# Kernel optimization log

Hardware: AMD Instinct MI355X
Metric: run time of the kernel (lower is better)

## Reference

```python
import jax, jax.numpy as jnp
import numpy as np

D_MODEL = 256
SEQ_L = 4096
BATCH = 8
H = 3 * D_MODEL   # inner width after 3-branch concat
N_STATE = 32      # complex conjugate pairs -> d_state=64 real
KSIZES = (3, 7, 15)
DILATIONS = (1, 2, 4)


def setup_inputs() -> dict:
    k = jax.random.split(jax.random.key(0), 16)
    d = D_MODEL
    def w(ki, shape, scale):
        return jax.random.normal(ki, shape, jnp.float32) * scale
    inp = {"x": jax.random.normal(k[0], (BATCH, SEQ_L, d), jnp.float32)}
    for i, ksz in enumerate(KSIZES):
        inp[f"conv_w{i}"] = w(k[1 + i], (d, d, ksz), (d * ksz) ** -0.5)
        inp[f"conv_b{i}"] = jnp.zeros((d,), jnp.float32)
    inp["gate_w"] = w(k[4], (H, d), d ** -0.5)
    inp["gate_b"] = jnp.zeros((H,), jnp.float32)
    inp["res_w"] = w(k[5], (H, d), d ** -0.5)
    inp["res_b"] = jnp.zeros((H,), jnp.float32)
    # S4D (diagonal SSM) parameters, d_state=64 -> 32 complex pairs
    inp["log_dt"] = jax.random.uniform(k[6], (H,), jnp.float32, np.log(0.001), np.log(0.1))
    inp["A_re"] = -0.5 * jnp.ones((H, N_STATE), jnp.float32)
    inp["A_im"] = jnp.broadcast_to(np.pi * jnp.arange(N_STATE, dtype=jnp.float32), (H, N_STATE)).copy()
    inp["C_re"] = w(k[7], (H, N_STATE), 0.2)
    inp["C_im"] = w(k[8], (H, N_STATE), 0.2)
    inp["Dskip"] = jax.random.normal(k[9], (H,), jnp.float32)
    inp["ln_gamma"] = jnp.ones((H,), jnp.float32)
    inp["ln_beta"] = jnp.zeros((H,), jnp.float32)
    return inp


def _dil_conv(u, w, b, dil):
    # u: [B, C, L], w: [O, I, K], torch 'same' padding (odd kernels)
    y = jax.lax.conv_general_dilated(
        u, w, window_strides=(1,), padding="SAME", rhs_dilation=(dil,),
        dimension_numbers=("NCH", "OIH", "NCH"))
    return y + b[None, :, None]


def _s4d_apply(u, log_dt, A_re, A_im, C_re, C_im, Dskip):
    # u: [B, H, L]; diagonal SSM long convolution via FFT (ZOH discretization)
    L = u.shape[-1]
    dt = jnp.exp(log_dt)                          # [H]
    A = A_re + 1j * A_im                          # [H, N]
    C = C_re + 1j * C_im                          # [H, N]
    dtA = dt[:, None] * A                         # [H, N]
    C_disc = C * (jnp.exp(dtA) - 1.0) / A         # ZOH input matrix folded into C
    t = jnp.arange(L, dtype=jnp.float32)
    vand = jnp.exp(dtA[:, :, None] * t)           # [H, N, L] Vandermonde
    kern = 2.0 * jnp.real(jnp.einsum("hn,hnl->hl", C_disc, vand))  # [H, L]
    n_fft = 2 * L
    kf = jnp.fft.rfft(kern, n_fft)                # [H, n_fft/2+1]
    uf = jnp.fft.rfft(u, n_fft)                   # [B, H, n_fft/2+1]
    y = jnp.fft.irfft(uf * kf[None], n_fft)[..., :L]
    return y + Dskip[None, :, None] * u


def reference(x, conv_w0, conv_b0, conv_w1, conv_b1, conv_w2, conv_b2,
              gate_w, gate_b, res_w, res_b,
              log_dt, A_re, A_im, C_re, C_im, Dskip, ln_gamma, ln_beta):
    u = jnp.transpose(x, (0, 2, 1))               # [B, d, L]
    convs = [
        _dil_conv(u, conv_w0, conv_b0, DILATIONS[0]),
        _dil_conv(u, conv_w1, conv_b1, DILATIONS[1]),
        _dil_conv(u, conv_w2, conv_b2, DILATIONS[2]),
    ]
    combined = jnp.concatenate(convs, axis=1)     # [B, 3d, L]
    gate = jax.nn.sigmoid(jnp.einsum("bdl,od->bol", u, gate_w) + gate_b[None, :, None])
    gated = combined * gate
    s4_out = _s4d_apply(gated, log_dt, A_re, A_im, C_re, C_im, Dskip)
    resid = jnp.einsum("bdl,od->bol", u, res_w) + res_b[None, :, None]
    out = jnp.transpose(s4_out + resid, (0, 2, 1))  # [B, L, 3d]
    mu = jnp.mean(out, axis=-1, keepdims=True)
    var = jnp.mean((out - mu) ** 2, axis=-1, keepdims=True)
    return (out - mu) * jax.lax.rsqrt(var + 1e-5) * ln_gamma + ln_beta
```

## Files before the change

### kernel.cpp

```cpp
#include <hip/hip_runtime.h>
#include <cstdint>
#include <cstddef>


#define B_ 8
#define L_ 4096
#define D_ 256
#define H_ 768
#define NST 32
#define LC 128
#define NC 32

typedef _Float16 f16;
typedef _Float16 f16x8 __attribute__((ext_vector_type(8)));
typedef _Float16 f16x4 __attribute__((ext_vector_type(4)));
typedef _Float16 f16x2 __attribute__((ext_vector_type(2)));
typedef float f32x4 __attribute__((ext_vector_type(4)));

__device__ __forceinline__ f32x4 mfma16(f16x8 a, f16x8 b, f32x4 c) {
  return __builtin_amdgcn_mfma_f32_16x16x32_f16(a, b, c, 0, 0, 0);
}

#define GLDS16(g, l)                                                              \
  __builtin_amdgcn_global_load_lds((const __attribute__((address_space(1))) void*)(g), \
                                   (__attribute__((address_space(3))) void*)(l), 16, 0, 0)

__global__ __launch_bounds__(256) void prep_all(
    const float* __restrict__ x, const float* __restrict__ gate_w,
    const float* __restrict__ res_w,
    const float* __restrict__ w0, const float* __restrict__ w1, const float* __restrict__ w2,
    f16* __restrict__ xh, f16* __restrict__ Ag, float* __restrict__ zbuf,
    f16* __restrict__ A) {
  int bid = blockIdx.x, tid = threadIdx.x;
  if (bid < 8192) {
    int i = (bid * 256 + tid) * 4;
    float4 v = *(const float4*)(x + i);
    xh[i+0]=(f16)v.x; xh[i+1]=(f16)v.y; xh[i+2]=(f16)v.z; xh[i+3]=(f16)v.w;
  } else if (bid < 8384) {
    int i = ((bid - 8192) * 256 + tid) * 4;
    float4 v = *(const float4*)(gate_w + i);
    Ag[i+0]=(f16)v.x; Ag[i+1]=(f16)v.y; Ag[i+2]=(f16)v.z; Ag[i+3]=(f16)v.w;
  } else if (bid < 8576) {
    int i = ((bid - 8384) * 256 + tid) * 4;
    float4 v = *(const float4*)(res_w + i);
    f16* d = Ag + 768 * 256;
    d[i+0]=(f16)v.x; d[i+1]=(f16)v.y; d[i+2]=(f16)v.z; d[i+3]=(f16)v.w;
  } else if (bid == 8576) {
    zbuf[tid] = 0.f;
  } else {
    int idx = (bid - 8577) * 256 + tid;
    const int n0 = 256 * 256 * 3, n1 = 256 * 256 * 7;
    const float* w; int K, base;
    if (idx < n0) { w = w0; K = 3; base = 0; }
    else if (idx < n0 + n1) { idx -= n0; w = w1; K = 7; base = 256 * 768; }
    else { idx -= n0 + n1; w = w2; K = 15; base = 256 * 768 + 256 * 1792; }
    int o = idx / (256 * K); int r = idx - o * (256 * K); int j = r / K; int t = r - j * K;
    A[base + o * (256 * K) + t * 256 + j] = (f16)w[idx];
  }
}

__global__ __launch_bounds__(256) void s4_all(const float* __restrict__ log_dt,
                                              const float* __restrict__ A_re,
                                              const float* __restrict__ A_im,
                                              const float* __restrict__ C_re,
                                              const float* __restrict__ C_im,
                                              f16* __restrict__ A1, f16* __restrict__ A2,
                                              float* __restrict__ WLc,
                                              float* __restrict__ kT) {
  int bid = blockIdx.x, tid = threadIdx.x;
  if (bid < 96) {
    int idx = bid * 256 + tid;
    int h = idx >> 5, n = idx & 31;
    float dt = expf(log_dt[h]);
    float Ar = A_re[idx], Ai = A_im[idx];
    float ar = dt * Ar, ai = dt * Ai;
    float e = expf(ar), sn, cs; sincosf(ai, &sn, &cs);
    float wr = e * cs, wi = e * sn;
    float den = Ar * Ar + Ai * Ai;
    float Er = wr - 1.f, Ei = wi;
    float Cr = C_re[idx], Ci = C_im[idx];
    float nr = Cr * Er - Ci * Ei, ni = Cr * Ei + Ci * Er;
    float Cdr = (nr * Ar + ni * Ai) / den;
    float Cdi = (ni * Ar - nr * Ai) / den;
    f16* A1r = A1 + ((size_t)h * 64 + 2 * n) * LC;
    f16* A1i = A1 + ((size_t)h * 64 + 2 * n + 1) * LC;
    float pr = 1.f, pi = 0.f;
    for (int j = 0; j < LC; ++j) {
      A1r[LC - 1 - j] = (f16)pr; A1i[LC - 1 - j] = (f16)pi;
      float t0 = pr * wr - pi * wi; pi = pr * wi + pi * wr; pr = t0;
    }
    WLc[idx * 2] = pr; WLc[idx * 2 + 1] = pi;
    float qr = wr, qi = wi;
    for (int t = 0; t < LC; ++t) {
      A2[((size_t)h * LC + t) * 64 + 2 * n]     = (f16)(2.f * (Cdr * qr - Cdi * qi));
      A2[((size_t)h * LC + t) * 64 + 2 * n + 1] = (f16)(-2.f * (Cdr * qi + Cdi * qr));
      float t0 = qr * wr - qi * wi; qi = qr * wi + qi * wr; qr = t0;
    }
  } else {
    int idx = (bid - 96) * 256 + tid;
    int h = idx >> 7, j = idx & 127;
    float dt = expf(log_dt[h]);
    float acc = 0.f;
    for (int n = 0; n < NST; ++n) {
      float Ar = A_re[h * 32 + n], Ai = A_im[h * 32 + n];
      float ar = dt * Ar, ai = dt * Ai;
      float e1 = expf(ar), s1, c1; sincosf(ai, &s1, &c1);
      float wr = e1 * c1, wi = e1 * s1;
      float den = Ar * Ar + Ai * Ai;
      float Er = wr - 1.f, Ei = wi;
      float Cr = C_re[h * 32 + n], Ci = C_im[h * 32 + n];
      float nr = Cr * Er - Ci * Ei, ni = Cr * Ei + Ci * Er;
      float Cdr = (nr * Ar + ni * Ai) / den, Cdi = (ni * Ar - nr * Ai) / den;
      float ej = expf(ar * (float)j), sj, cj; sincosf(ai * (float)j, &sj, &cj);
      acc += 2.f * (Cdr * (ej * cj) - Cdi * (ej * sj));
    }
    kT[idx] = acc;
  }
}

__global__ __launch_bounds__(256) void gemm_gr(
    const f16* __restrict__ xh, const f16* __restrict__ Agr,
    const float* __restrict__ gate_b, const float* __restrict__ res_b,
    f16* __restrict__ gts, f16* __restrict__ res) {
  __shared__ f16 As[128 * 64];
  __shared__ f16 Bs[128 * 64];
  const int mt = blockIdx.y, nt = blockIdx.x;
  const int b = nt >> 5, l0 = (nt & 31) * 128;
  const bool isg = mt < 6;
  const int hbase = (isg ? mt : mt - 6) * 128;
  const f16* Abase = Agr + (size_t)((isg ? 0 : 768) + hbase) * 256;
  const int tid = threadIdx.x;
  const int wid = tid >> 6, lane = tid & 63, l15 = lane & 15, quad = lane >> 4;
  const int wm = (wid & 1) * 64, wn = (wid >> 1) * 64;
  const int srow = (wid << 5) + (lane >> 3);
  const int sperm = ((lane & 7) ^ (lane >> 3)) << 3;
  char* AsL = (char*)As + (wid << 12);
  char* BsL = (char*)Bs + (wid << 12);
  const f16* xrow = xh + (((size_t)b * L_) << 8);

  f32x4 acc[4][4];
#pragma unroll
  for (int i = 0; i < 4; ++i)
#pragma unroll
    for (int j = 0; j < 4; ++j) acc[i][j] = (f32x4){0.f, 0.f, 0.f, 0.f};

  for (int kc = 0; kc < 4; ++kc) {
#pragma unroll
    for (int j = 0; j < 4; ++j) {
      int row = srow + j * 8;
      GLDS16(Abase + (size_t)row * 256 + kc * 64 + sperm, AsL + (j << 10));
      GLDS16(xrow + ((size_t)(l0 + row) << 8) + kc * 64 + sperm, BsL + (j << 10));
    }
    __syncthreads();
#pragma unroll
    for (int k2 = 0; k2 < 2; ++k2) {
      f16x8 af[4], bf[4];
#pragma unroll
      for (int mi = 0; mi < 4; ++mi) {
        int r = wm + mi * 16 + l15;
        af[mi] = *(const f16x8*)(&As[r * 64 + (((k2 * 4 + quad) ^ (r & 7)) << 3)]);
      }
#pragma unroll
      for (int ni = 0; ni < 4; ++ni) {
        int r = wn + ni * 16 + l15;
        bf[ni] = *(const f16x8*)(&Bs[r * 64 + (((k2 * 4 + quad) ^ (r & 7)) << 3)]);
      }
#pragma unroll
      for (int mi = 0; mi < 4; ++mi)
#pragma unroll
        for (int ni = 0; ni < 4; ++ni) acc[mi][ni] = mfma16(af[mi], bf[ni], acc[mi][ni]);
    }
    __syncthreads();
  }

  if (isg) {
#pragma unroll
    for (int mi = 0; mi < 4; ++mi)
#pragma unroll
      for (int ni = 0; ni < 4; ++ni) {
        int hg = hbase + wm + mi * 16 + quad * 4;
        int lg = l0 + wn + ni * 16 + l15;
#pragma unroll
        for (int r = 0; r < 4; ++r) {
          float val = acc[mi][ni][r] + gate_b[hg + r];
          gts[((size_t)(b * H_ + hg + r)) * L_ + lg] = (f16)(1.f / (1.f + expf(-val)));
        }
      }
  } else {
#pragma unroll
    for (int mi = 0; mi < 4; ++mi)
#pragma unroll
      for (int ni = 0; ni < 4; ++ni) {
        int hg = hbase + wm + mi * 16 + quad * 4;
        int lg = l0 + wn + ni * 16 + l15;
#pragma unroll
        for (int r = 0; r < 4; ++r)
          res[((size_t)(b * H_ + hg + r)) * L_ + lg] = (f16)(acc[mi][ni][r] + res_b[hg + r]);
      }
  }
}

__global__ __launch_bounds__(512, 2) void gemm_conv8(
    const f16* __restrict__ xh, const f16* __restrict__ Aconv,
    const float* __restrict__ cb0, const float* __restrict__ cb1, const float* __restrict__ cb2,
    const f16* __restrict__ gts, const f16* __restrict__ zbuf,
    f16* __restrict__ v) {
  __shared__ f16 lds[65536];
  f16* A0 = lds;
  f16* B0 = lds + 16384;
  f16* A1 = lds + 32768;
  f16* B1 = lds + 49152;

  const int nt = blockIdx.x;
  const int b = nt >> 4, l0 = (nt & 15) * 256;
  const int ci = 2 - blockIdx.y;
  const int tid = threadIdx.x;
  const int wid = tid >> 6, lane = tid & 63, l15 = lane & 15, quad = lane >> 4;
  const int wr = wid >> 2, wc = wid & 3;
  const int r0 = tid >> 3;
  const int cswz = ((tid & 7) ^ ((tid >> 3) & 7)) << 3;
  const int rsw = lane & 7;
  const f16* xrow = xh + (((size_t)b * L_) << 8);

  const f16* Acb; int Krow, taps, dil;
  if (ci == 0)      { Acb = Aconv;                          Krow = 768;  taps = 3;  dil = 1; }
  else if (ci == 1) { Acb = Aconv + 256 * 768;              Krow = 1792; taps = 7;  dil = 2; }
  else              { Acb = Aconv + 256 * 768 + 256 * 1792; Krow = 3840; taps = 15; dil = 4; }
  const int KS = taps * 4;

  f32x4 acc[8][4];
#pragma unroll
  for (int i = 0; i < 8; ++i)
#pragma unroll
    for (int j = 0; j < 4; ++j) acc[i][j] = (f32x4){0.f, 0.f, 0.f, 0.f};
  f16x8 af[4][2], blo[2][2], bhi[2][2];

  auto stageA = [&](int kst, int h, f16* Ad) {
    int t = kst >> 2, jb = (kst & 3) << 6;
    const f16* s0 = Acb + (size_t)(h * 128 + r0) * Krow + t * 256 + jb + cswz;
    GLDS16(s0, Ad + h * 8192 + wid * 512);
    GLDS16(s0 + (size_t)64 * Krow, Ad + h * 8192 + 4096 + wid * 512);
  };
  auto stageB = [&](int kst, int h, f16* Bd) {
    int t = kst >> 2, jb = (kst & 3) << 6;
    int boff = (t - (taps - 1) / 2) * dil;
    int gl0 = l0 + h * 128 + r0 + boff;
    const f16* s0 = (gl0 < 0 || gl0 >= L_) ? (zbuf + cswz)
                    : xrow + ((size_t)gl0 << 8) + jb + cswz;
    GLDS16(s0, Bd + h * 8192 + wid * 512);
    int gl1 = gl0 + 64;
    const f16* s1 = (gl1 < 0 || gl1 >= L_) ? (zbuf + cswz)
                    : xrow + ((size_t)gl1 << 8) + jb + cswz;
    GLDS16(s1, Bd + h * 8192 + 4096 + wid * 512);
  };
  auto loadA = [&](const f16* Ab, int MH) {
#pragma unroll
    for (int mi = 0; mi < 4; ++mi) {
      int r = MH * 128 + wr * 64 + mi * 16 + l15;
#pragma unroll
      for (int k2 = 0; k2 < 2; ++k2)
        af[mi][k2] = *(const f16x8*)(Ab + r * 64 + (((k2 * 4 + quad) ^ rsw) << 3));
    }
  };
  auto loadB = [&](const f16* Bb, int NH, f16x8 (&bf)[2][2]) {
#pragma unroll
    for (int ni = 0; ni < 2; ++ni) {
      int r = NH * 128 + wc * 32 + ni * 16 + l15;
#pragma unroll
      for (int k2 = 0; k2 < 2; ++k2)
        bf[ni][k2] = *(const f16x8*)(Bb + r * 64 + (((k2 * 4 + quad) ^ rsw) << 3));
    }
  };
  auto quadMM = [&](int MH, int NH, f16x8 (&bf)[2][2]) {
#pragma unroll
    for (int k2 = 0; k2 < 2; ++k2)
#pragma unroll
      for (int mi = 0; mi < 4; ++mi)
#pragma unroll
        for (int ni = 0; ni < 2; ++ni)
          acc[MH * 4 + mi][NH * 2 + ni] =
              mfma16(af[mi][k2], bf[ni][k2], acc[MH * 4 + mi][NH * 2 + ni]);
  };

  auto kstep = [&](int kst, f16* Ab, f16* Bb, f16* AbN, f16* BbN) {
    loadA(Ab, 0); loadB(Bb, 0, blo);
    if (kst + 1 < KS) stageB(kst + 1, 0, BbN);
    __builtin_amdgcn_s_barrier();
    asm volatile("s_waitcnt lgkmcnt(0)" ::: "memory");
    __builtin_amdgcn_s_setprio(1);
    quadMM(0, 0, blo);
    __builtin_amdgcn_s_setprio(0);
    __builtin_amdgcn_s_barrier();
    loadB(Bb, 1, bhi);
    if (kst + 1 < KS) stageA(kst + 1, 1, AbN);
    __builtin_amdgcn_s_barrier();
    asm volatile("s_waitcnt lgkmcnt(0)" ::: "memory");
    __builtin_amdgcn_s_setprio(1);
    quadMM(0, 1, bhi);
    __builtin_amdgcn_s_setprio(0);
    __builtin_amdgcn_s_barrier();
    loadA(Ab, 1);
    if (kst + 2 < KS) stageA(kst + 2, 0, Ab);
    __builtin_amdgcn_s_barrier();
    asm volatile("s_waitcnt lgkmcnt(0)" ::: "memory");
    __builtin_amdgcn_s_setprio(1);
    quadMM(1, 1, bhi);
    __builtin_amdgcn_s_setprio(0);
    __builtin_amdgcn_s_barrier();
    if (kst + 2 < KS) stageB(kst + 2, 1, Bb);
    __builtin_amdgcn_s_barrier();
    asm volatile("s_waitcnt lgkmcnt(0)" ::: "memory");
    __builtin_amdgcn_s_setprio(1);
    quadMM(1, 0, blo);
    __builtin_amdgcn_s_setprio(0);
    if (kst + 2 < KS) asm volatile("s_waitcnt vmcnt(4)" ::: "memory");
    else              asm volatile("s_waitcnt vmcnt(0)" ::: "memory");
    __builtin_amdgcn_s_barrier();
  };

  stageA(0, 0, A0);
  stageB(0, 1, B0);
  stageB(0, 0, B0);
  stageA(0, 1, A0);
  stageA(1, 0, A1);
  stageB(1, 1, B1);
  asm volatile("s_waitcnt vmcnt(4)" ::: "memory");
  __builtin_amdgcn_s_barrier();

#pragma unroll 1
  for (int k = 0; k < KS; k += 2) {
    kstep(k,     A0, B0, A1, B1);
    kstep(k + 1, A1, B1, A0, B0);
  }

  const float* cbias = (ci == 0) ? cb0 : (ci == 1 ? cb1 : cb2);
#pragma unroll
  for (int mh = 0; mh < 2; ++mh)
#pragma unroll
    for (int mi = 0; mi < 4; ++mi)
#pragma unroll
      for (int nh = 0; nh < 2; ++nh)
#pragma unroll
        for (int ni = 0; ni < 2; ++ni) {
          int mg = mh * 128 + wr * 64 + mi * 16 + quad * 4;
          int lg = l0 + nh * 128 + wc * 32 + ni * 16 + l15;
          f32x4 a4 = acc[mh * 4 + mi][nh * 2 + ni];
#pragma unroll
          for (int r = 0; r < 4; ++r) {
            size_t a = ((size_t)(b * H_ + ci * 256 + mg + r)) * L_ + lg;
            float val = (a4[r] + cbias[mg + r]) * (float)gts[a];
            v[a] = (f16)val;
          }
        }
}

__global__ __launch_bounds__(256) void s1_states(const f16* __restrict__ v,
                                                 const f16* __restrict__ A1,
                                                 const float* __restrict__ WLc,
                                                 f16* __restrict__ Xin) {
  __shared__ f16 A1s[64 * 136];
  __shared__ f16 Vs[128 * 136];
  const int h = blockIdx.y, cb = blockIdx.x;
  const int tid = threadIdx.x;
  {
    int row = tid >> 2, q = tid & 3;
    const f16x8* src = (const f16x8*)(A1 + ((size_t)h * 64 + row) * 128 + q * 32);
    f16x8* dst = (f16x8*)(&A1s[row * 136 + q * 32]);
    dst[0] = src[0]; dst[1] = src[1]; dst[2] = src[2]; dst[3] = src[3];
  }
  {
    int col = tid >> 1, half = tid & 1;
    int cg = cb * 128 + col, b = cg >> 5, c = cg & 31;
    const f16x8* src = (const f16x8*)(v + ((size_t)(b * H_ + h)) * L_ + c * 128 + half * 64);
    f16x8* dst = (f16x8*)(&Vs[col * 136 + half * 64]);
    dst[0] = src[0]; dst[1] = src[1]; dst[2] = src[2]; dst[3] = src[3];
    dst[4] = src[4]; dst[5] = src[5]; dst[6] = src[6]; dst[7] = src[7];
  }
  __syncthreads();
  const int wid = tid >> 6, lane = tid & 63, l15 = lane & 15, quad = lane >> 4;
  const int n0 = wid * 32;
  f32x4 acc[4][2];
#pragma unroll
  for (int i = 0; i < 4; ++i) { acc[i][0] = (f32x4){0,0,0,0}; acc[i][1] = (f32x4){0,0,0,0}; }
#pragma unroll
  for (int bk = 0; bk < 4; ++bk) {
    f16x8 af[4], bf[2];
#pragma unroll
    for (int mi = 0; mi < 4; ++mi)
      af[mi] = *(const f16x8*)(&A1s[(mi * 16 + l15) * 136 + bk * 32 + quad * 8]);
#pragma unroll
    for (int ni = 0; ni < 2; ++ni)
      bf[ni] = *(const f16x8*)(&Vs[(n0 + ni * 16 + l15) * 136 + bk * 32 + quad * 8]);
#pragma unroll
    for (int mi = 0; mi < 4; ++mi)
#pragma unroll
      for (int ni = 0; ni < 2; ++ni) acc[mi][ni] = mfma16(af[mi], bf[ni], acc[mi][ni]);
  }
  __syncthreads();
  float* Xls = (float*)Vs;
#pragma unroll
  for (int mi = 0; mi < 4; ++mi)
#pragma unroll
    for (int ni = 0; ni < 2; ++ni) {
      int col = n0 + ni * 16 + l15;
      *(f32x4*)(&Xls[col * 68 + mi * 16 + quad * 4]) = acc[mi][ni];
    }
  __syncthreads();
  if (tid < 128) {
    int b4 = tid >> 5, n = tid & 31;
    int b = cb * 4 + b4;
    float Wr = WLc[(h * NST + n) * 2], Wi = WLc[(h * NST + n) * 2 + 1];
    float xr = 0.f, xi = 0.f;
    f16* xout = Xin + (((size_t)(b * H_ + h)) * NC) * 64 + 2 * n;
    for (int c = 0; c < NC; ++c) {
      float er = Xls[(b4 * 32 + c) * 68 + 2 * n];
      float ei = Xls[(b4 * 32 + c) * 68 + 2 * n + 1];
      f16x2 o; o[0] = (f16)xr; o[1] = (f16)xi;
      *(f16x2*)(xout + (size_t)c * 64) = o;
      float t = Wr * xr - Wi * xi + er;
      xi = Wr * xi + Wi * xr + ei; xr = t;
    }
  }
}

__global__ __launch_bounds__(256) void s3_output(const f16* __restrict__ v,
                                                 const f16* __restrict__ A2g,
                                                 const f16* __restrict__ res,
                                                 const float* __restrict__ kT,
                                                 const f16* __restrict__ Xin,
                                                 const float* __restrict__ Dskip,
                                                 f16* __restrict__ y4) {
  __shared__ f16 Ts[128 * 136];
  __shared__ f16 Vs[64 * 136];
  __shared__ float kTs[128];
  f16* A2s = Ts;
  f16* Xs = Ts + 128 * 72;
  const int h = blockIdx.y, cb = blockIdx.x;
  const int tid = threadIdx.x;
  if (tid < 128) kTs[tid] = kT[h * 128 + tid];
  {
    int col = tid >> 2, q = tid & 3;
    int cg = cb * 64 + col, b = cg >> 5, c = cg & 31;
    const f16x8* src = (const f16x8*)(v + ((size_t)(b * H_ + h)) * L_ + c * 128 + q * 32);
    f16x8* dst = (f16x8*)(&Vs[col * 136 + q * 32]);
    dst[0] = src[0]; dst[1] = src[1]; dst[2] = src[2]; dst[3] = src[3];
  }
  __syncthreads();
  {
    int tau = tid >> 1, h64 = (tid & 1) * 64;
#pragma unroll
    for (int jv = 0; jv < 8; ++jv) {
      int s0 = h64 + jv * 8;
      f16x8 w;
#pragma unroll
      for (int e = 0; e < 8; ++e) {
        int s = s0 + e;
        w[e] = (f16)((s <= tau) ? kTs[tau - s] : 0.f);
      }
      *(f16x8*)(&Ts[tau * 136 + s0]) = w;
    }
  }
  __syncthreads();
  const int wid = tid >> 6, lane = tid & 63, l15 = lane & 15, quad = lane >> 4;
  const int wm = (wid & 1) * 64, wn = (wid >> 1) * 32;
  f32x4 acc[4][2];
#pragma unroll
  for (int i = 0; i < 4; ++i) { acc[i][0] = (f32x4){0,0,0,0}; acc[i][1] = (f32x4){0,0,0,0}; }
#pragma unroll
  for (int bk = 0; bk < 4; ++bk) {
    f16x8 af[4], bf[2];
#pragma unroll
    for (int mi = 0; mi < 4; ++mi)
      af[mi] = *(const f16x8*)(&Ts[(wm + mi * 16 + l15) * 136 + bk * 32 + quad * 8]);
#pragma unroll
    for (int ni = 0; ni < 2; ++ni)
      bf[ni] = *(const f16x8*)(&Vs[(wn + ni * 16 + l15) * 136 + bk * 32 + quad * 8]);
#pragma unroll
    for (int mi = 0; mi < 4; ++mi)
#pragma unroll
      for (int ni = 0; ni < 2; ++ni) acc[mi][ni] = mfma16(af[mi], bf[ni], acc[mi][ni]);
  }
  __syncthreads();
  {
    int row = tid >> 1, half = tid & 1;
    const f16x8* src = (const f16x8*)(A2g + ((size_t)h * 128 + row) * 64 + half * 32);
    f16x8* dst = (f16x8*)(&A2s[row * 72 + half * 32]);
    dst[0] = src[0]; dst[1] = src[1]; dst[2] = src[2]; dst[3] = src[3];
  }
  {
    int col = tid >> 2, part = tid & 3;
    int cg = cb * 64 + col, b = cg >> 5, c = cg & 31;
    const f16x8* src = (const f16x8*)(Xin + (((size_t)(b * H_ + h)) * NC + c) * 64 + part * 16);
    f16x8* dst = (f16x8*)(&Xs[col * 72 + part * 16]);
    dst[0] = src[0]; dst[1] = src[1];
  }
  __syncthreads();
#pragma unroll
  for (int bk = 0; bk < 2; ++bk) {
    f16x8 af[4], bf[2];
#pragma unroll
    for (int mi = 0; mi < 4; ++mi)
      af[mi] = *(const f16x8*)(&A2s[(wm + mi * 16 + l15) * 72 + bk * 32 + quad * 8]);
#pragma unroll
    for (int ni = 0; ni < 2; ++ni)
      bf[ni] = *(const f16x8*)(&Xs[(wn + ni * 16 + l15) * 72 + bk * 32 + quad * 8]);
#pragma unroll
    for (int mi = 0; mi < 4; ++mi)
#pragma unroll
      for (int ni = 0; ni < 2; ++ni) acc[mi][ni] = mfma16(af[mi], bf[ni], acc[mi][ni]);
  }
  float Dh = Dskip[h];
#pragma unroll
  for (int mi = 0; mi < 4; ++mi)
#pragma unroll
    for (int ni = 0; ni < 2; ++ni) {
      int col = wn + ni * 16 + l15;
      int cg = cb * 64 + col, b = cg >> 5, c = cg & 31;
      int tau0 = wm + mi * 16 + quad * 4;
      size_t lbase = ((size_t)(b * H_ + h)) * L_ + c * 128 + tau0;
      const f16* rp = res + lbase;
      f16x4 o;
#pragma unroll
      for (int r = 0; r < 4; ++r)
        o[r] = (f16)(acc[mi][ni][r] + Dh * (float)Vs[col * 136 + tau0 + r] + (float)rp[r]);
      *(f16x4*)(y4 + lbase) = o;
    }
}

__global__ __launch_bounds__(256) void layernorm_t(const f16* __restrict__ y4,
                                                   const float* __restrict__ gamma,
                                                   const float* __restrict__ beta,
                                                   float* __restrict__ out) {
  __shared__ f16 Ys[768 * 72];
  __shared__ float psum[256], psq[256], mu[64], rs[64];
  const int b = blockIdx.y, l0 = blockIdx.x * 64;
  const int tid = threadIdx.x;
  {
    int r8 = tid >> 3, c = tid & 7;
    for (int it = 0; it < 24; ++it) {
      int hh = it * 32 + r8;
      f16x8 x = *(const f16x8*)(y4 + ((size_t)(b * H_ + hh)) * L_ + l0 + c * 8);
      *(f16x8*)(&Ys[hh * 72 + c * 8]) = x;
    }
  }
  __syncthreads();
  {
    int l = tid & 63, hg = tid >> 6;
    float s = 0.f, s2 = 0.f;
    for (int k = 0; k < 192; ++k) {
      float val = (float)Ys[(hg * 192 + k) * 72 + l];
      s += val; s2 += val * val;
    }
    psum[hg * 64 + l] = s; psq[hg * 64 + l] = s2;
  }
  __syncthreads();
  if (tid < 64) {
    float S = 0.f, S2 = 0.f;
    for (int g = 0; g < 4; ++g) { S += psum[g * 64 + tid]; S2 += psq[g * 64 + tid]; }
    float m = S / 768.f;
    float var = S2 / 768.f - m * m;
    mu[tid] = m; rs[tid] = rsqrtf(var + 1e-5f);
  }
  __syncthreads();
  float g0 = gamma[tid], g1 = gamma[256 + tid], g2 = gamma[512 + tid];
  float be0 = beta[tid], be1 = beta[256 + tid], be2 = beta[512 + tid];
  for (int lv = 0; lv < 8; ++lv) {
    f16x8 y0 = *(const f16x8*)(&Ys[(size_t)tid * 72 + lv * 8]);
    f16x8 y1 = *(const f16x8*)(&Ys[(size_t)(256 + tid) * 72 + lv * 8]);
    f16x8 y2 = *(const f16x8*)(&Ys[(size_t)(512 + tid) * 72 + lv * 8]);
#pragma unroll
    for (int e = 0; e < 8; ++e) {
      int ll = lv * 8 + e;
      float m = mu[ll], r = rs[ll];
      size_t ob = ((size_t)b * L_ + l0 + ll) * H_;
      out[ob + tid]       = ((float)y0[e] - m) * r * g0 + be0;
      out[ob + 256 + tid] = ((float)y1[e] - m) * r * g1 + be1;
      out[ob + 512 + tid] = ((float)y2[e] - m) * r * g2 + be2;
    }
  }
}

extern "C" void kernel_launch(void* const* d_in, const int* in_sizes, int n_in,
                              void* d_out, int out_size, void* d_ws, size_t ws_size,
                              hipStream_t stream) {
  const float* x      = (const float*)d_in[0];
  const float* cw0    = (const float*)d_in[1];
  const float* cb0    = (const float*)d_in[2];
  const float* cw1    = (const float*)d_in[3];
  const float* cb1    = (const float*)d_in[4];
  const float* cw2    = (const float*)d_in[5];
  const float* cb2    = (const float*)d_in[6];
  const float* gate_w = (const float*)d_in[7];
  const float* gate_b = (const float*)d_in[8];
  const float* res_w  = (const float*)d_in[9];
  const float* res_b  = (const float*)d_in[10];
  const float* log_dt = (const float*)d_in[11];
  const float* A_re   = (const float*)d_in[12];
  const float* A_im   = (const float*)d_in[13];
  const float* C_re   = (const float*)d_in[14];
  const float* C_im   = (const float*)d_in[15];
  const float* Dskip  = (const float*)d_in[16];
  const float* ln_g   = (const float*)d_in[17];
  const float* ln_b   = (const float*)d_in[18];
  float* out = (float*)d_out;

  char* ws = (char*)d_ws;
  f16*   xh   = (f16*)(ws + 0);
  f16*   Ac   = (f16*)(ws + 16777216);
  f16*   Ag   = (f16*)(ws + 20054016);
  f16*   zbuf = (f16*)(ws + 20840448);
  f16*   vb   = (f16*)(ws + 20841472);
  f16*   resb = (f16*)(ws + 71173120);
  f16*   gts  = (f16*)(ws + 121504768);
  f16*   A1   = (f16*)(ws + 171836416);
  f16*   A2   = (f16*)(ws + 184419328);
  float* kT   = (float*)(ws + 197002240);
  float* WLc  = (float*)(ws + 197395456);
  f16*   Xin  = (f16*)(ws + 197592064);
  f16*   y4   = (f16*)(ws + 222757888);

  prep_all<<<14977, 256, 0, stream>>>(x, gate_w, res_w, cw0, cw1, cw2,
                                      xh, Ag, (float*)zbuf, Ac);
  s4_all<<<480, 256, 0, stream>>>(log_dt, A_re, A_im, C_re, C_im, A1, A2, WLc, kT);

  gemm_gr<<<dim3(256, 12), 256, 0, stream>>>(xh, Ag, gate_b, res_b, gts, resb);
  gemm_conv8<<<dim3(128, 3), 512, 0, stream>>>(xh, Ac, cb0, cb1, cb2, gts, zbuf, vb);

  s1_states<<<dim3(2, 768), 256, 0, stream>>>(vb, A1, WLc, Xin);
  s3_output<<<dim3(4, 768), 256, 0, stream>>>(vb, A2, resb, kT, Xin, Dskip, y4);

  layernorm_t<<<dim3(64, 8), 256, 0, stream>>>(y4, ln_g, ln_b, out);
}
```

Before: 458.9 us.

## Reuse one staged x halo tile across all conv taps per channel chunk

```diff
diff --git a/kernel.cpp b/kernel.cpp
--- a/kernel.cpp
+++ b/kernel.cpp
@@ -205,11 +205,8 @@
     const float* __restrict__ cb0, const float* __restrict__ cb1, const float* __restrict__ cb2,
     const f16* __restrict__ gts, const f16* __restrict__ zbuf,
     f16* __restrict__ v) {
-  __shared__ f16 lds[65536];
-  f16* A0 = lds;
-  f16* B0 = lds + 16384;
-  f16* A1 = lds + 32768;
-  f16* B1 = lds + 49152;
+  __shared__ f16 lds[69632];
+  f16* Bs = lds + 49152;
 
   const int nt = blockIdx.x;
   const int b = nt >> 4, l0 = (nt & 15) * 256;
@@ -217,16 +214,16 @@
   const int tid = threadIdx.x;
   const int wid = tid >> 6, lane = tid & 63, l15 = lane & 15, quad = lane >> 4;
   const int wr = wid >> 2, wc = wid & 3;
-  const int r0 = tid >> 3;
+  const int rq = tid >> 3;
   const int cswz = ((tid & 7) ^ ((tid >> 3) & 7)) << 3;
-  const int rsw = lane & 7;
   const f16* xrow = xh + (((size_t)b * L_) << 8);
 
   const f16* Acb; int Krow, taps, dil;
   if (ci == 0)      { Acb = Aconv;                          Krow = 768;  taps = 3;  dil = 1; }
   else if (ci == 1) { Acb = Aconv + 256 * 768;              Krow = 1792; taps = 7;  dil = 2; }
   else              { Acb = Aconv + 256 * 768 + 256 * 1792; Krow = 3840; taps = 15; dil = 4; }
-  const int KS = taps * 4;
+  const int S = taps * 4;
+  const int half = (taps - 1) / 2;
 
   f32x4 acc[8][4];
 #pragma unroll
@@ -235,23 +232,22 @@
     for (int j = 0; j < 4; ++j) acc[i][j] = (f32x4){0.f, 0.f, 0.f, 0.f};
   f16x8 af[4][2], blo[2][2], bhi[2][2];
 
-  auto stageA = [&](int kst, int h, f16* Ad) {
-    int t = kst >> 2, jb = (kst & 3) << 6;
-    const f16* s0 = Acb + (size_t)(h * 128 + r0) * Krow + t * 256 + jb + cswz;
-    GLDS16(s0, Ad + h * 8192 + wid * 512);
-    GLDS16(s0 + (size_t)64 * Krow, Ad + h * 8192 + 4096 + wid * 512);
+  auto stageB = [&](int jc) {
+#pragma unroll
+    for (int q = 0; q < 5; ++q) {
+      int r = q * 64 + rq;
+      int gl = l0 - 32 + r;
+      const f16* src = (gl < 0 || gl >= L_) ? (zbuf + cswz)
+                       : xrow + ((size_t)gl << 8) + jc * 64 + cswz;
+      GLDS16(src, Bs + q * 4096 + wid * 512);
+    }
   };
-  auto stageB = [&](int kst, int h, f16* Bd) {
-    int t = kst >> 2, jb = (kst & 3) << 6;
-    int boff = (t - (taps - 1) / 2) * dil;
-    int gl0 = l0 + h * 128 + r0 + boff;
-    const f16* s0 = (gl0 < 0 || gl0 >= L_) ? (zbuf + cswz)
-                    : xrow + ((size_t)gl0 << 8) + jb + cswz;
-    GLDS16(s0, Bd + h * 8192 + wid * 512);
-    int gl1 = gl0 + 64;
-    const f16* s1 = (gl1 < 0 || gl1 >= L_) ? (zbuf + cswz)
-                    : xrow + ((size_t)gl1 << 8) + jb + cswz;
-    GLDS16(s1, Bd + h * 8192 + 4096 + wid * 512);
+  auto stageA2 = [&](int t2, int jc2, f16* buf, int q0) {
+#pragma unroll
+    for (int q = q0; q < q0 + 2; ++q) {
+      const f16* src = Acb + (size_t)(q * 64 + rq) * Krow + t2 * 256 + jc2 * 64 + cswz;
+      GLDS16(src, buf + q * 4096 + wid * 512);
+    }
   };
   auto loadA = [&](const f16* Ab, int MH) {
 #pragma unroll
@@ -259,16 +255,16 @@
       int r = MH * 128 + wr * 64 + mi * 16 + l15;
 #pragma unroll
       for (int k2 = 0; k2 < 2; ++k2)
-        af[mi][k2] = *(const f16x8*)(Ab + r * 64 + (((k2 * 4 + quad) ^ rsw) << 3));
+        af[mi][k2] = *(const f16x8*)(Ab + r * 64 + (((k2 * 4 + quad) ^ (r & 7)) << 3));
     }
   };
-  auto loadB = [&](const f16* Bb, int NH, f16x8 (&bf)[2][2]) {
+  auto loadB = [&](int NH, int shift, f16x8 (&bf)[2][2]) {
 #pragma unroll
     for (int ni = 0; ni < 2; ++ni) {
-      int r = NH * 128 + wc * 32 + ni * 16 + l15;
+      int r = shift + NH * 128 + wc * 32 + ni * 16 + l15;
 #pragma unroll
       for (int k2 = 0; k2 < 2; ++k2)
-        bf[ni][k2] = *(const f16x8*)(Bb + r * 64 + (((k2 * 4 + quad) ^ rsw) << 3));
+        bf[ni][k2] = *(const f16x8*)(Bs + r * 64 + (((k2 * 4 + quad) ^ (r & 7)) << 3));
     }
   };
   auto quadMM = [&](int MH, int NH, f16x8 (&bf)[2][2]) {
@@ -282,55 +278,60 @@
               mfma16(af[mi][k2], bf[ni][k2], acc[MH * 4 + mi][NH * 2 + ni]);
   };
 
-  auto kstep = [&](int kst, f16* Ab, f16* Bb, f16* AbN, f16* BbN) {
-    loadA(Ab, 0); loadB(Bb, 0, blo);
-    if (kst + 1 < KS) stageB(kst + 1, 0, BbN);
-    __builtin_amdgcn_s_barrier();
-    asm volatile("s_waitcnt lgkmcnt(0)" ::: "memory");
-    __builtin_amdgcn_s_setprio(1);
-    quadMM(0, 0, blo);
-    __builtin_amdgcn_s_setprio(0);
-    __builtin_amdgcn_s_barrier();
-    loadB(Bb, 1, bhi);
-    if (kst + 1 < KS) stageA(kst + 1, 1, AbN);
-    __builtin_amdgcn_s_barrier();
-    asm volatile("s_waitcnt lgkmcnt(0)" ::: "memory");
-    __builtin_amdgcn_s_setprio(1);
-    quadMM(0, 1, bhi);
-    __builtin_amdgcn_s_setprio(0);
-    __builtin_amdgcn_s_barrier();
-    loadA(Ab, 1);
-    if (kst + 2 < KS) stageA(kst + 2, 0, Ab);
-    __builtin_amdgcn_s_barrier();
-    asm volatile("s_waitcnt lgkmcnt(0)" ::: "memory");
-    __builtin_amdgcn_s_setprio(1);
-    quadMM(1, 1, bhi);
-    __builtin_amdgcn_s_setprio(0);
-    __builtin_amdgcn_s_barrier();
-    if (kst + 2 < KS) stageB(kst + 2, 1, Bb);
-    __builtin_amdgcn_s_barrier();
-    asm volatile("s_waitcnt lgkmcnt(0)" ::: "memory");
-    __builtin_amdgcn_s_setprio(1);
-    quadMM(1, 0, blo);
-    __builtin_amdgcn_s_setprio(0);
-    if (kst + 2 < KS) asm volatile("s_waitcnt vmcnt(4)" ::: "memory");
-    else              asm volatile("s_waitcnt vmcnt(0)" ::: "memory");
-    __builtin_amdgcn_s_barrier();
-  };
-
-  stageA(0, 0, A0);
-  stageB(0, 1, B0);
-  stageB(0, 0, B0);
-  stageA(0, 1, A0);
-  stageA(1, 0, A1);
-  stageB(1, 1, B1);
-  asm volatile("s_waitcnt vmcnt(4)" ::: "memory");
+  stageB(0);
+  stageA2(0, 0, lds, 0);           stageA2(0, 0, lds, 2);
+  stageA2(1, 0, lds + 16384, 0);   stageA2(1, 0, lds + 16384, 2);
+  asm volatile("s_waitcnt vmcnt(0)" ::: "memory");
   __builtin_amdgcn_s_barrier();
 
+  int s = 0, ca = 0;
 #pragma unroll 1
-  for (int k = 0; k < KS; k += 2) {
-    kstep(k,     A0, B0, A1, B1);
-    kstep(k + 1, A1, B1, A0, B0);
+  for (int jc = 0; jc < 4; ++jc) {
+    if (jc > 0) {
+      stageB(jc);
+      asm volatile("s_waitcnt vmcnt(0)" ::: "memory");
+      __builtin_amdgcn_s_barrier();
+    }
+#pragma unroll 1
+    for (int t = 0; t < taps; ++t, ++s) {
+      const int shift = 32 + (t - half) * dil;
+      f16* Acur = lds + ca * 16384;
+      int pa = ca - 1; if (pa < 0) pa = 2;
+      f16* Apre = lds + pa * 16384;
+      int t2 = t + 2, jc2 = jc;
+      if (t2 >= taps) { t2 -= taps; ++jc2; }
+      const bool pf = (jc2 < 4);
+      loadA(Acur, 0); loadB(0, shift, blo);
+      if (pf) stageA2(t2, jc2, Apre, 0);
+      __builtin_amdgcn_s_barrier();
+      asm volatile("s_waitcnt lgkmcnt(0)" ::: "memory");
+      __builtin_amdgcn_s_setprio(1);
+      quadMM(0, 0, blo);
+      __builtin_amdgcn_s_setprio(0);
+      __builtin_amdgcn_s_barrier();
+      loadB(1, shift, bhi);
+      if (pf) stageA2(t2, jc2, Apre, 2);
+      __builtin_amdgcn_s_barrier();
+      asm volatile("s_waitcnt lgkmcnt(0)" ::: "memory");
+      __builtin_amdgcn_s_setprio(1);
+      quadMM(0, 1, bhi);
+      __builtin_amdgcn_s_setprio(0);
+      __builtin_amdgcn_s_barrier();
+      loadA(Acur, 1);
+      __builtin_amdgcn_s_barrier();
+      asm volatile("s_waitcnt lgkmcnt(0)" ::: "memory");
+      __builtin_amdgcn_s_setprio(1);
+      quadMM(1, 1, bhi);
+      __builtin_amdgcn_s_setprio(0);
+      __builtin_amdgcn_s_barrier();
+      __builtin_amdgcn_s_setprio(1);
+      quadMM(1, 0, blo);
+      __builtin_amdgcn_s_setprio(0);
+      if (pf) asm volatile("s_waitcnt vmcnt(4)" ::: "memory");
+      else    asm volatile("s_waitcnt vmcnt(0)" ::: "memory");
+      __builtin_amdgcn_s_barrier();
+      ca = (ca == 2) ? 0 : ca + 1;
+    }
   }
 
   const float* cbias = (ci == 0) ? cb0 : (ci == 1 ? cb1 : cb2);
```

Measured after the change: 453.6 us. About the same (-1.1%).
